# Optimization experiments

Hardware: AMD Instinct MI355X
Metric: run time of the kernel (lower is better)

## Reference

```python
import jax, jax.numpy as jnp
import numpy as np

N_NODES = 50000
N_EDGES = 800000
F_IN, F_HID, F_OUT = 128, 256, 128


def setup_inputs() -> dict:
    key = jax.random.key(0)
    ks = jax.random.split(key, 16)
    inp = {
        "x": jax.random.normal(ks[0], (N_NODES, F_IN), dtype=jnp.float32),
        "edge0": jax.random.randint(ks[1], (2, N_EDGES), 0, N_NODES, dtype=jnp.int64),
        "edge1": jax.random.randint(ks[2], (2, N_EDGES), 0, N_NODES, dtype=jnp.int64),
        "edge2": jax.random.randint(ks[3], (2, N_EDGES), 0, N_NODES, dtype=jnp.int64),
    }
    dims = [(F_IN, F_HID), (F_HID, F_HID), (F_HID, F_OUT)]
    for i, (di, do) in enumerate(dims):
        inp[f"Wl{i}"] = 0.02 * jax.random.normal(ks[4 + 3 * i], (di, do), dtype=jnp.float32)
        inp[f"bl{i}"] = jnp.zeros((do,), dtype=jnp.float32)
        inp[f"Wr{i}"] = 0.02 * jax.random.normal(ks[5 + 3 * i], (di, do), dtype=jnp.float32)
    return inp


def _sage_layer(x, src, dst, Wl, bl, Wr):
    # gather source features, mean-aggregate into destinations
    msg = x[src]                                            # [E, F]
    agg = jax.ops.segment_sum(msg, dst, num_segments=N_NODES)
    cnt = jax.ops.segment_sum(jnp.ones((src.shape[0], 1), x.dtype), dst,
                              num_segments=N_NODES)
    mean = agg / jnp.maximum(cnt, 1.0)
    # PyG SAGEConv: lin_l(aggr) + lin_r(x_self); lin_r has no bias
    return mean @ Wl + bl + x @ Wr


def reference(x, edge0, edge1, edge2, Wl0, bl0, Wr0, Wl1, bl1, Wr1, Wl2, bl2, Wr2):
    # vstack-swap + flow='target_to_source' == aggregate edge[0] -> edge[1]
    edges = [edge0, edge1, edge2]
    params = [(Wl0, bl0, Wr0), (Wl1, bl1, Wr1), (Wl2, bl2, Wr2)]
    h = x
    for e, (Wl, bl, Wr) in zip(edges, params):
        h = _sage_layer(h, e[0], e[1], Wl, bl, Wr)
        h = jax.nn.relu(h)
        # dropout skipped (eval mode)
    return h
```

## Files before the change

### kernel.cpp

```cpp
#include <hip/hip_runtime.h>
#include <hip/hip_bf16.h>
#include <stdint.h>

#define N_NODES 50000
#define N_EDGES 800000
#define NBG 196
#define MG 3125
#define MG64 782
#define EG 3125

typedef __attribute__((ext_vector_type(8))) short short8;
typedef __attribute__((ext_vector_type(4))) float floatx4;

__device__ __forceinline__ float bfbits2f(unsigned int u16) {
    union { unsigned int i; float f; } c; c.i = u16 << 16; return c.f;
}
__device__ __forceinline__ unsigned short f2bfbits(float f) {
    union { float f; unsigned int i; } c; c.f = f;
    unsigned int r = c.i + 0x7fffu + ((c.i >> 16) & 1u);
    return (unsigned short)(r >> 16);
}
__device__ __forceinline__ void acc8(float* a, uint4 v) {
    a[0] += bfbits2f(v.x & 0xffffu); a[1] += bfbits2f(v.x >> 16);
    a[2] += bfbits2f(v.y & 0xffffu); a[3] += bfbits2f(v.y >> 16);
    a[4] += bfbits2f(v.z & 0xffffu); a[5] += bfbits2f(v.z >> 16);
    a[6] += bfbits2f(v.w & 0xffffu); a[7] += bfbits2f(v.w >> 16);
}

__device__ __forceinline__ void count_body(
    int i, const int* __restrict__ e, int* __restrict__ rp, int f1)
{
    int dst = f1 ? e[2 * (N_EDGES + i)] : e[N_EDGES + i];
    atomicAdd(&rp[dst], 1);
}

__device__ __forceinline__ void fill_body(
    int i, const int* __restrict__ e, int* __restrict__ rp,
    const int* __restrict__ part, int* __restrict__ csr, int f1)
{
    int src = f1 ? e[2 * i] : e[i];
    int dst = f1 ? e[2 * (N_EDGES + i)] : e[N_EDGES + i];
    int pos = part[dst >> 8] + atomicAdd(&rp[dst], 1);
    csr[pos] = src;
}

__global__ __launch_bounds__(256) void mega1(
    const void* __restrict__ Wl0, const void* __restrict__ Wr0,
    const void* __restrict__ Wl1, const void* __restrict__ Wr1,
    const void* __restrict__ Wl2, const void* __restrict__ Wr2,
    const void* __restrict__ b0, const void* __restrict__ b1, const void* __restrict__ b2,
    unsigned short* __restrict__ wt,
    const void* __restrict__ x, unsigned short* __restrict__ xb,
    const int* __restrict__ e0,
    int* __restrict__ rp0, int* __restrict__ flagsOut)
{
    __shared__ int s_cnt[2];
    const int t = threadIdx.x;
    if (t < 2) s_cnt[t] = 0;
    __syncthreads();
    {
        unsigned short v = ((const unsigned short*)x)[2 * t];
        int ex = (v >> 7) & 0xff;
        unsigned long long m0 = __ballot(v == 0 || (ex >= 96 && ex <= 150));
        unsigned long long m1 = __ballot(e0[2 * t + 1] != 0);
        if ((t & 63) == 0) {
            atomicAdd(&s_cnt[0], (int)__popcll(m0));
            atomicAdd(&s_cnt[1], (int)__popcll(m1));
        }
    }
    __syncthreads();
    const int f0 = (s_cnt[0] < 200) ? 1 : 0;
    const int f1 = (s_cnt[1] < 128) ? 1 : 0;
    const int bid = blockIdx.x;

    if (bid == 10402) {
        if (t == 0) { flagsOut[0] = f0; flagsOut[1] = f1; }
        return;
    }
    if (bid >= 7277) {
        count_body((bid - 7277) * 256 + t, e0, rp0, f1);
        return;
    }
    if (bid >= 1027) {
        int i = (bid - 1027) * 256 + t;
        if (f0) {
            float4 v = ((const float4*)x)[i];
            uint2 o;
            o.x = (unsigned int)f2bfbits(v.x) | ((unsigned int)f2bfbits(v.y) << 16);
            o.y = (unsigned int)f2bfbits(v.z) | ((unsigned int)f2bfbits(v.w) << 16);
            ((uint2*)xb)[i] = o;
        } else {
            ((uint2*)xb)[i] = ((const uint2*)x)[i];
        }
        return;
    }
    if (bid >= 1024) {
        const void* bs = bid == 1024 ? b0 : (bid == 1025 ? b1 : b2);
        unsigned short* bd = wt + 262144 + (bid - 1024) * 256;
        int n = (bid == 1026) ? 128 : 256;
        if (t < n) bd[t] = f0 ? f2bfbits(((const float*)bs)[t]) : ((const unsigned short*)bs)[t];
        return;
    }
    const void* W; unsigned short* WT; int Nd, SK, KO, off;
    if (bid < 128)      { W = Wl0; WT = wt;          Nd = 256; off = bid;       SK = 256; KO = 0;   }
    else if (bid < 256) { W = Wr0; WT = wt;          Nd = 256; off = bid - 128; SK = 256; KO = 128; }
    else if (bid < 512) { W = Wl1; WT = wt + 65536;  Nd = 256; off = bid - 256; SK = 512; KO = 0;   }
    else if (bid < 768) { W = Wr1; WT = wt + 65536;  Nd = 256; off = bid - 512; SK = 512; KO = 256; }
    else if (bid < 896) { W = Wl2; WT = wt + 196608; Nd = 128; off = bid - 768; SK = 256; KO = 0;   }
    else                { W = Wr2; WT = wt + 229376; Nd = 128; off = bid - 896; SK = 256; KO = 0;   }
    int idx = off * 256 + t;
    int k = idx / Nd, n = idx - k * Nd;
    unsigned short v = f0 ? f2bfbits(((const float*)W)[idx]) : ((const unsigned short*)W)[idx];
    WT[n * SK + KO + k] = v;
}

__global__ __launch_bounds__(256) void scan_g(
    int* __restrict__ rp, int* __restrict__ part, int* __restrict__ ticket)
{
    __shared__ int sa[256], sb[256];
    __shared__ int lastBlk;
    const int b = blockIdx.x, t = threadIdx.x, idx = b * 256 + t;
    int v = (idx < N_NODES) ? rp[idx] : 0;
    sa[t] = v;
    __syncthreads();
    bool par = true;
#pragma unroll
    for (int off = 1; off < 256; off <<= 1) {
        if (par) { int x2 = sa[t] + (t >= off ? sa[t - off] : 0); sb[t] = x2; }
        else     { int x2 = sb[t] + (t >= off ? sb[t - off] : 0); sa[t] = x2; }
        par = !par;
        __syncthreads();
    }
    if (idx < N_NODES) rp[idx] = sa[t] - v;
    if (t == 255) part[b] = sa[255];
    __threadfence();
    if (t == 0) lastBlk = (atomicAdd(ticket, 1) == (int)gridDim.x - 1) ? 1 : 0;
    __syncthreads();
    if (!lastBlk) return;

    int pv = (t < NBG) ? atomicAdd(&part[t], 0) : 0;
    sa[t] = pv;
    __syncthreads();
    par = true;
#pragma unroll
    for (int off = 1; off < 256; off <<= 1) {
        if (par) { int x2 = sa[t] + (t >= off ? sa[t - off] : 0); sb[t] = x2; }
        else     { int x2 = sb[t] + (t >= off ? sb[t - off] : 0); sa[t] = x2; }
        par = !par;
        __syncthreads();
    }
    if (t < NBG) part[t] = sa[t] - pv;
}

__global__ __launch_bounds__(256) void fill_k(
    const int* __restrict__ e, int* __restrict__ rp, const int* __restrict__ part,
    int* __restrict__ csr, const int* __restrict__ flags)
{
    fill_body(blockIdx.x * 256 + threadIdx.x, e, rp, part, csr, flags[1]);
}

template<int K, int OSTR>
__global__ __launch_bounds__(256) void gath(
    const unsigned short* __restrict__ hin,
    const int* __restrict__ rp, const int* __restrict__ part,
    const int* __restrict__ csr_src,
    unsigned short* __restrict__ mout,
    const int* __restrict__ eN, int* __restrict__ rpN,
    const int* __restrict__ flags)
{
    constexpr int CH = K / 8;
    constexpr int CAP = 1024;
    __shared__ int sidx[CAP];
    __shared__ int srp[17];
    const int tid = threadIdx.x;
    if (blockIdx.x >= MG) {
        count_body((blockIdx.x - MG) * 256 + tid, eN, rpN, flags[1]);
        return;
    }
    const int m0 = blockIdx.x * 16;
    if (tid < 17) {
        int r0 = m0 + tid - 1;
        srp[tid] = (r0 < 0) ? 0 : rp[r0] + part[r0 >> 8];
    }
    __syncthreads();
    const int base = srp[0];
    const int total = srp[16] - base;
    const bool staged = total <= CAP;
    if (staged) {
        for (int i = tid; i < total; i += 256) sidx[i] = csr_src[base + i];
    }
    __syncthreads();

    for (int it = tid; it < 16 * CH; it += 256) {
        const int rr = it / CH;
        const int cc = it & (CH - 1);
        const int beg = srp[rr];
        const int deg = srp[rr + 1] - beg;
        const int begl = beg - base;
        float a[8], g[8];
#pragma unroll
        for (int v = 0; v < 8; ++v) { a[v] = 0.f; g[v] = 0.f; }
        const unsigned short* col = hin + cc * 8;
        auto run = [&](auto IDX) {
            int j = 0;
            for (; j + 7 < deg; j += 8) {
                int s0 = IDX(j),     s1 = IDX(j + 1), s2 = IDX(j + 2), s3 = IDX(j + 3);
                int s4 = IDX(j + 4), s5 = IDX(j + 5), s6 = IDX(j + 6), s7 = IDX(j + 7);
                uint4 v0 = *(const uint4*)(col + (size_t)s0 * K);
                uint4 v1 = *(const uint4*)(col + (size_t)s1 * K);
                uint4 v2 = *(const uint4*)(col + (size_t)s2 * K);
                uint4 v3 = *(const uint4*)(col + (size_t)s3 * K);
                uint4 v4 = *(const uint4*)(col + (size_t)s4 * K);
                uint4 v5 = *(const uint4*)(col + (size_t)s5 * K);
                uint4 v6 = *(const uint4*)(col + (size_t)s6 * K);
                uint4 v7 = *(const uint4*)(col + (size_t)s7 * K);
                acc8(a, v0); acc8(g, v1); acc8(a, v2); acc8(g, v3);
                acc8(a, v4); acc8(g, v5); acc8(a, v6); acc8(g, v7);
            }
            for (; j + 1 < deg; j += 2) {
                int s0 = IDX(j), s1 = IDX(j + 1);
                uint4 v0 = *(const uint4*)(col + (size_t)s0 * K);
                uint4 v1 = *(const uint4*)(col + (size_t)s1 * K);
                acc8(a, v0); acc8(g, v1);
            }
            if (j < deg) {
                uint4 v0 = *(const uint4*)(col + (size_t)IDX(j) * K);
                acc8(a, v0);
            }
        };
        if (staged) run([&](int j) { return sidx[begl + j]; });
        else        run([&](int j) { return csr_src[beg + j]; });
        const float inv = 1.0f / fmaxf((float)deg, 1.0f);
        short8 t8;
#pragma unroll
        for (int v = 0; v < 8; ++v) t8[v] = (short)f2bfbits((a[v] + g[v]) * inv);
        *(short8*)(mout + (size_t)(m0 + rr) * OSTR + cc * 8) = t8;
    }
}

template<int K>
__global__ __launch_bounds__(256) void gemmcat(
    const unsigned short* __restrict__ mean, int mstr,
    const unsigned short* __restrict__ self, int sstr,
    const unsigned short* __restrict__ WcatT,
    const unsigned short* __restrict__ bb,
    unsigned short* __restrict__ hout,
    const int* __restrict__ ef, int* __restrict__ rpf, const int* __restrict__ partf,
    int* __restrict__ csr, const int* __restrict__ flags)
{
    constexpr int KE = 2 * K;
    constexpr int KH = 256;
    constexpr int NKH = KE / KH;
    constexpr int LDA = KH + 8;
    __shared__ unsigned short A[64][LDA];
    const int tid = threadIdx.x;
    if (blockIdx.x >= MG64) {
        fill_body((blockIdx.x - MG64) * 256 + tid, ef, rpf, partf, csr, flags[1]);
        return;
    }
    const int m0 = blockIdx.x * 64;
    const int lane = tid & 63, wave = tid >> 6;
    const int r = lane & 15, quad = lane >> 4;

    floatx4 acc[4][4] = {};

#pragma unroll
    for (int kh = 0; kh < NKH; ++kh) {
        if (kh) __syncthreads();
        for (int i = tid; i < 64 * (KH / 8); i += 256) {
            const int row = i / (KH / 8);
            const int c8 = i - row * (KH / 8);
            int grow = m0 + row; if (grow >= N_NODES) grow = N_NODES - 1;
            const int gc = kh * KH + c8 * 8;
            const unsigned short* src = (gc < K)
                ? (mean + (size_t)grow * mstr + gc)
                : (self + (size_t)grow * sstr + (gc - K));
            *(uint4*)&A[row][c8 * 8] = *(const uint4*)src;
        }
        __syncthreads();
#pragma unroll
        for (int nti = 0; nti < 4; ++nti) {
            const int n0 = (wave + nti * 4) * 16;
            short8 bf[KH / 32];
            const unsigned short* bp = WcatT + (size_t)(n0 + r) * KE + kh * KH + quad * 8;
#pragma unroll
            for (int k0 = 0; k0 < KH / 32; ++k0) bf[k0] = *(const short8*)(bp + k0 * 32);
#pragma unroll
            for (int mt = 0; mt < 4; ++mt) {
#pragma unroll
                for (int k0 = 0; k0 < KH / 32; ++k0)
                    acc[nti][mt] = __builtin_amdgcn_mfma_f32_16x16x32_bf16(
                        *(const short8*)&A[mt * 16 + r][k0 * 32 + quad * 8],
                        bf[k0], acc[nti][mt], 0, 0, 0);
            }
        }
    }

#pragma unroll
    for (int nti = 0; nti < 4; ++nti) {
        const int ccol = (wave + nti * 4) * 16 + r;
        const float bv = bfbits2f(bb[ccol]);
#pragma unroll
        for (int mt = 0; mt < 4; ++mt) {
#pragma unroll
            for (int i = 0; i < 4; ++i) {
                const int row = m0 + mt * 16 + quad * 4 + i;
                float v = acc[nti][mt][i] + bv;
                v = v > 0.f ? v : 0.f;
                if (row < N_NODES) hout[(size_t)row * 256 + ccol] = f2bfbits(v);
            }
        }
    }
}

__global__ __launch_bounds__(256) void gemmL2(
    const unsigned short* __restrict__ A,
    const unsigned short* __restrict__ WT,
    unsigned short* __restrict__ out0,
    unsigned short* __restrict__ out1)
{
    __shared__ unsigned short As[64][264];
    const int tid = threadIdx.x;
    const int m0 = blockIdx.x * 64;
    for (int i = tid; i < 64 * 32; i += 256) {
        int rr = i >> 5, cc = i & 31;
        int row = m0 + rr; if (row >= N_NODES) row = N_NODES - 1;
        *(uint4*)&As[rr][cc * 8] = *(const uint4*)(A + (size_t)row * 256 + cc * 8);
    }
    __syncthreads();
    const int lane = tid & 63, wave = tid >> 6;
    const int r = lane & 15, quad = lane >> 4;

    for (int nt = wave; nt < 16; nt += 4) {
        const int n0 = nt * 16;
        short8 bf[8];
        const unsigned short* bp = WT + (size_t)(n0 + r) * 256 + quad * 8;
#pragma unroll
        for (int k0 = 0; k0 < 8; ++k0) bf[k0] = *(const short8*)(bp + k0 * 32);
        const int ccol = n0 + r;
#pragma unroll
        for (int mt = 0; mt < 4; ++mt) {
            floatx4 acc = {0.f, 0.f, 0.f, 0.f};
#pragma unroll
            for (int k0 = 0; k0 < 8; ++k0)
                acc = __builtin_amdgcn_mfma_f32_16x16x32_bf16(
                    *(const short8*)&As[mt * 16 + r][k0 * 32 + quad * 8], bf[k0], acc, 0, 0, 0);
#pragma unroll
            for (int i = 0; i < 4; ++i) {
                const int row = m0 + mt * 16 + quad * 4 + i;
                if (row < N_NODES) {
                    unsigned short v = f2bfbits(acc[i]);
                    if (ccol < 128) out0[(size_t)row * 128 + ccol] = v;
                    else            out1[(size_t)row * 128 + ccol - 128] = v;
                }
            }
        }
    }
}

__global__ __launch_bounds__(256) void agg2(
    const unsigned short* __restrict__ hl2,
    const unsigned short* __restrict__ hr2,
    const int* __restrict__ rp, const int* __restrict__ part,
    const int* __restrict__ csr_src,
    const unsigned short* __restrict__ bb,
    void* __restrict__ out,
    const int* __restrict__ flags)
{
    constexpr int K = 128, CAP = 3072;
    __shared__ int sidx[CAP];
    __shared__ int srp[17];
    const int tid = threadIdx.x;
    const int m0 = blockIdx.x * 16;
    if (tid < 17) {
        int r0 = m0 + tid - 1;
        srp[tid] = (r0 < 0) ? 0 : rp[r0] + part[r0 >> 8];
    }
    __syncthreads();
    const int base = srp[0];
    const int total = srp[16] - base;
    const bool staged = total <= CAP;
    if (staged) {
        for (int i = tid; i < total; i += 256) sidx[i] = csr_src[base + i];
    }
    __syncthreads();

    const int rr = tid >> 4;
    const int cc = tid & 15;
    const int beg = srp[rr];
    const int deg = srp[rr + 1] - beg;
    const int begl = beg - base;
    float a[8], g[8];
#pragma unroll
    for (int v = 0; v < 8; ++v) { a[v] = 0.f; g[v] = 0.f; }
    const unsigned short* col = hl2 + cc * 8;
    auto run = [&](auto IDX) {
        int j = 0;
        for (; j + 7 < deg; j += 8) {
            int s0 = IDX(j),     s1 = IDX(j + 1), s2 = IDX(j + 2), s3 = IDX(j + 3);
            int s4 = IDX(j + 4), s5 = IDX(j + 5), s6 = IDX(j + 6), s7 = IDX(j + 7);
            uint4 v0 = *(const uint4*)(col + (size_t)s0 * K);
            uint4 v1 = *(const uint4*)(col + (size_t)s1 * K);
            uint4 v2 = *(const uint4*)(col + (size_t)s2 * K);
            uint4 v3 = *(const uint4*)(col + (size_t)s3 * K);
            uint4 v4 = *(const uint4*)(col + (size_t)s4 * K);
            uint4 v5 = *(const uint4*)(col + (size_t)s5 * K);
            uint4 v6 = *(const uint4*)(col + (size_t)s6 * K);
            uint4 v7 = *(const uint4*)(col + (size_t)s7 * K);
            acc8(a, v0); acc8(g, v1); acc8(a, v2); acc8(g, v3);
            acc8(a, v4); acc8(g, v5); acc8(a, v6); acc8(g, v7);
        }
        for (; j + 1 < deg; j += 2) {
            int s0 = IDX(j), s1 = IDX(j + 1);
            uint4 v0 = *(const uint4*)(col + (size_t)s0 * K);
            uint4 v1 = *(const uint4*)(col + (size_t)s1 * K);
            acc8(a, v0); acc8(g, v1);
        }
        if (j < deg) {
            uint4 v0 = *(const uint4*)(col + (size_t)IDX(j) * K);
            acc8(a, v0);
        }
    };
    if (staged) run([&](int j) { return sidx[begl + j]; });
    else        run([&](int j) { return csr_src[beg + j]; });

    const float inv = 1.0f / fmaxf((float)deg, 1.0f);
    const size_t ro = (size_t)(m0 + rr) * K + cc * 8;
    uint4 hv = *(const uint4*)(hr2 + ro);
    uint4 bv = *(const uint4*)(bb + cc * 8);
    float h8[8], b8[8];
    h8[0] = bfbits2f(hv.x & 0xffffu); h8[1] = bfbits2f(hv.x >> 16);
    h8[2] = bfbits2f(hv.y & 0xffffu); h8[3] = bfbits2f(hv.y >> 16);
    h8[4] = bfbits2f(hv.z & 0xffffu); h8[5] = bfbits2f(hv.z >> 16);
    h8[6] = bfbits2f(hv.w & 0xffffu); h8[7] = bfbits2f(hv.w >> 16);
    b8[0] = bfbits2f(bv.x & 0xffffu); b8[1] = bfbits2f(bv.x >> 16);
    b8[2] = bfbits2f(bv.y & 0xffffu); b8[3] = bfbits2f(bv.y >> 16);
    b8[4] = bfbits2f(bv.z & 0xffffu); b8[5] = bfbits2f(bv.z >> 16);
    b8[6] = bfbits2f(bv.w & 0xffffu); b8[7] = bfbits2f(bv.w >> 16);
    float o8[8];
#pragma unroll
    for (int v = 0; v < 8; ++v) {
        float m = (a[v] + g[v]) * inv + b8[v] + h8[v];
        o8[v] = m > 0.f ? m : 0.f;
    }
    if (flags[0]) {
        float* op = (float*)out + ro;
        float4 o0 = { o8[0], o8[1], o8[2], o8[3] };
        float4 o1 = { o8[4], o8[5], o8[6], o8[7] };
        *(float4*)op = o0;
        *(float4*)(op + 4) = o1;
    } else {
        short8 t8;
#pragma unroll
        for (int v = 0; v < 8; ++v) t8[v] = (short)f2bfbits(o8[v]);
        *(short8*)((unsigned short*)out + ro) = t8;
    }
}

extern "C" void kernel_launch(void* const* d_in, const int* in_sizes, int n_in,
                              void* d_out, int out_size, void* d_ws, size_t ws_size,
                              hipStream_t stream) {
    const void* x  = d_in[0];
    const int* e[3] = { (const int*)d_in[1], (const int*)d_in[2], (const int*)d_in[3] };

    char* ws = (char*)d_ws;
    int* flags = (int*)ws;
    unsigned short* wt = (unsigned short*)(ws + 1024);
    unsigned short* bb0 = wt + 262144;
    unsigned short* bb1 = wt + 262400;
    unsigned short* bb2 = wt + 262656;
    int* rp3    = (int*)(ws + 526592);
    int* ticket = (int*)(ws + 1126592);
    int* part3  = (int*)(ws + 1126604);
    int* csr    = (int*)(ws + 1128960);
    unsigned short* hA = (unsigned short*)(ws + 4328960);
    unsigned short* hB = (unsigned short*)(ws + 29928960);
    unsigned short* xb  = hB;
    unsigned short* hl2 = hA;
    unsigned short* hr2 = hA + (size_t)N_NODES * 128;

    int* rp0 = rp3, * rp1 = rp3 + N_NODES, * rp2 = rp3 + 2 * N_NODES;
    int* pt0 = part3, * pt1 = part3 + NBG, * pt2 = part3 + 2 * NBG;

    hipMemsetAsync(rp3, 0, 600012, stream);
    mega1<<<10403, 256, 0, stream>>>(d_in[4], d_in[6], d_in[7], d_in[9],
                                     d_in[10], d_in[12], d_in[5], d_in[8], d_in[11],
                                     wt, x, xb, e[0], rp0, flags);
    scan_g<<<NBG, 256, 0, stream>>>(rp0, pt0, ticket + 0);
    fill_k<<<EG, 256, 0, stream>>>(e[0], rp0, pt0, csr, flags);
    gath<128, 256><<<MG + EG, 256, 0, stream>>>(xb, rp0, pt0, csr, hA,
                                                e[1], rp1, flags);
    scan_g<<<NBG, 256, 0, stream>>>(rp1, pt1, ticket + 1);
    gemmcat<128><<<MG64 + EG, 256, 0, stream>>>(hA, 256, xb, 128,
                                                wt, bb0, hA,
                                                e[1], rp1, pt1, csr, flags);
    gath<256, 256><<<MG + EG, 256, 0, stream>>>(hA, rp1, pt1, csr, hB,
                                                e[2], rp2, flags);
    scan_g<<<NBG, 256, 0, stream>>>(rp2, pt2, ticket + 2);
    gemmcat<256><<<MG64 + EG, 256, 0, stream>>>(hB, 256, hA, 256,
                                                wt + 65536, bb1, hB,
                                                e[2], rp2, pt2, csr, flags);
    gemmL2<<<MG64, 256, 0, stream>>>(hB, wt + 196608, hl2, hr2);
    agg2<<<MG, 256, 0, stream>>>(hl2, hr2, rp2, pt2, csr, bb2, d_out, flags);
}
```

Measured before the change: 593.0 us.

## Coarsen edge count/fill blocks to four edges per thread and front-load them

The side-work that builds the edge histogram and CSR now handles four edges per thread, which cuts those block counts from 3125 to 782. In the fused gather and GEMM kernels, these blocks are moved to the start of the grid so they are dispatched first and overlap with the main work. The GEMM A-tile K chunk is also halved from 256 to 128, which shrinks LDS use and may raise occupancy at the cost of more synchronisation steps. Fewer, heavier atomic-issuing blocks lower scheduling overhead but may reduce latency hiding.

```diff
diff --git a/kernel.cpp b/kernel.cpp
--- a/kernel.cpp
+++ b/kernel.cpp
@@ -7,7 +7,7 @@
 #define NBG 196
 #define MG 3125
 #define MG64 782
-#define EG 3125
+#define EG4 782
 
 typedef __attribute__((ext_vector_type(8))) short short8;
 typedef __attribute__((ext_vector_type(4))) float floatx4;
@@ -27,21 +27,33 @@
     a[6] += bfbits2f(v.w & 0xffffu); a[7] += bfbits2f(v.w >> 16);
 }
 
-__device__ __forceinline__ void count_body(
-    int i, const int* __restrict__ e, int* __restrict__ rp, int f1)
-{
-    int dst = f1 ? e[2 * (N_EDGES + i)] : e[N_EDGES + i];
-    atomicAdd(&rp[dst], 1);
-}
-
-__device__ __forceinline__ void fill_body(
-    int i, const int* __restrict__ e, int* __restrict__ rp,
+__device__ __forceinline__ void count4_body(
+    int blk, int tid, const int* __restrict__ e, int* __restrict__ rp, int f1)
+{
+#pragma unroll
+    for (int u = 0; u < 4; ++u) {
+        int i = blk * 1024 + u * 256 + tid;
+        if (i < N_EDGES) {
+            int dst = f1 ? e[2 * (N_EDGES + i)] : e[N_EDGES + i];
+            atomicAdd(&rp[dst], 1);
+        }
+    }
+}
+
+__device__ __forceinline__ void fill4_body(
+    int blk, int tid, const int* __restrict__ e, int* __restrict__ rp,
     const int* __restrict__ part, int* __restrict__ csr, int f1)
 {
-    int src = f1 ? e[2 * i] : e[i];
-    int dst = f1 ? e[2 * (N_EDGES + i)] : e[N_EDGES + i];
-    int pos = part[dst >> 8] + atomicAdd(&rp[dst], 1);
-    csr[pos] = src;
+#pragma unroll
+    for (int u = 0; u < 4; ++u) {
+        int i = blk * 1024 + u * 256 + tid;
+        if (i < N_EDGES) {
+            int src = f1 ? e[2 * i] : e[i];
+            int dst = f1 ? e[2 * (N_EDGES + i)] : e[N_EDGES + i];
+            int pos = part[dst >> 8] + atomicAdd(&rp[dst], 1);
+            csr[pos] = src;
+        }
+    }
 }
 
 __global__ __launch_bounds__(256) void mega1(
@@ -73,12 +85,12 @@
     const int f1 = (s_cnt[1] < 128) ? 1 : 0;
     const int bid = blockIdx.x;
 
-    if (bid == 10402) {
+    if (bid == 8059) {
         if (t == 0) { flagsOut[0] = f0; flagsOut[1] = f1; }
         return;
     }
     if (bid >= 7277) {
-        count_body((bid - 7277) * 256 + t, e0, rp0, f1);
+        count4_body(bid - 7277, t, e0, rp0, f1);
         return;
     }
     if (bid >= 1027) {
@@ -156,7 +168,7 @@
     const int* __restrict__ e, int* __restrict__ rp, const int* __restrict__ part,
     int* __restrict__ csr, const int* __restrict__ flags)
 {
-    fill_body(blockIdx.x * 256 + threadIdx.x, e, rp, part, csr, flags[1]);
+    fill4_body(blockIdx.x, threadIdx.x, e, rp, part, csr, flags[1]);
 }
 
 template<int K, int OSTR>
@@ -173,11 +185,11 @@
     __shared__ int sidx[CAP];
     __shared__ int srp[17];
     const int tid = threadIdx.x;
-    if (blockIdx.x >= MG) {
-        count_body((blockIdx.x - MG) * 256 + tid, eN, rpN, flags[1]);
+    if (blockIdx.x < EG4) {
+        count4_body(blockIdx.x, tid, eN, rpN, flags[1]);
         return;
     }
-    const int m0 = blockIdx.x * 16;
+    const int m0 = (blockIdx.x - EG4) * 16;
     if (tid < 17) {
         int r0 = m0 + tid - 1;
         srp[tid] = (r0 < 0) ? 0 : rp[r0] + part[r0 >> 8];
@@ -249,16 +261,16 @@
     int* __restrict__ csr, const int* __restrict__ flags)
 {
     constexpr int KE = 2 * K;
-    constexpr int KH = 256;
+    constexpr int KH = 128;
     constexpr int NKH = KE / KH;
     constexpr int LDA = KH + 8;
     __shared__ unsigned short A[64][LDA];
     const int tid = threadIdx.x;
-    if (blockIdx.x >= MG64) {
-        fill_body((blockIdx.x - MG64) * 256 + tid, ef, rpf, partf, csr, flags[1]);
+    if (blockIdx.x < EG4) {
+        fill4_body(blockIdx.x, tid, ef, rpf, partf, csr, flags[1]);
         return;
     }
-    const int m0 = blockIdx.x * 64;
+    const int m0 = (blockIdx.x - EG4) * 64;
     const int lane = tid & 63, wave = tid >> 6;
     const int r = lane & 15, quad = lane >> 4;
 
@@ -483,23 +495,23 @@
     int* pt0 = part3, * pt1 = part3 + NBG, * pt2 = part3 + 2 * NBG;
 
     hipMemsetAsync(rp3, 0, 600012, stream);
-    mega1<<<10403, 256, 0, stream>>>(d_in[4], d_in[6], d_in[7], d_in[9],
-                                     d_in[10], d_in[12], d_in[5], d_in[8], d_in[11],
-                                     wt, x, xb, e[0], rp0, flags);
+    mega1<<<8060, 256, 0, stream>>>(d_in[4], d_in[6], d_in[7], d_in[9],
+                                    d_in[10], d_in[12], d_in[5], d_in[8], d_in[11],
+                                    wt, x, xb, e[0], rp0, flags);
     scan_g<<<NBG, 256, 0, stream>>>(rp0, pt0, ticket + 0);
-    fill_k<<<EG, 256, 0, stream>>>(e[0], rp0, pt0, csr, flags);
-    gath<128, 256><<<MG + EG, 256, 0, stream>>>(xb, rp0, pt0, csr, hA,
-                                                e[1], rp1, flags);
+    fill_k<<<EG4, 256, 0, stream>>>(e[0], rp0, pt0, csr, flags);
+    gath<128, 256><<<EG4 + MG, 256, 0, stream>>>(xb, rp0, pt0, csr, hA,
+                                                 e[1], rp1, flags);
     scan_g<<<NBG, 256, 0, stream>>>(rp1, pt1, ticket + 1);
-    gemmcat<128><<<MG64 + EG, 256, 0, stream>>>(hA, 256, xb, 128,
-                                                wt, bb0, hA,
-                                                e[1], rp1, pt1, csr, flags);
-    gath<256, 256><<<MG + EG, 256, 0, stream>>>(hA, rp1, pt1, csr, hB,
-                                                e[2], rp2, flags);
+    gemmcat<128><<<EG4 + MG64, 256, 0, stream>>>(hA, 256, xb, 128,
+                                                 wt, bb0, hA,
+                                                 e[1], rp1, pt1, csr, flags);
+    gath<256, 256><<<EG4 + MG, 256, 0, stream>>>(hA, rp1, pt1, csr, hB,
+                                                 e[2], rp2, flags);
     scan_g<<<NBG, 256, 0, stream>>>(rp2, pt2, ticket + 2);
-    gemmcat<256><<<MG64 + EG, 256, 0, stream>>>(hB, 256, hA, 256,
-                                                wt + 65536, bb1, hB,
-                                                e[2], rp2, pt2, csr, flags);
+    gemmcat<256><<<EG4 + MG64, 256, 0, stream>>>(hB, 256, hA, 256,
+                                                 wt + 65536, bb1, hB,
+                                                 e[2], rp2, pt2, csr, flags);
     gemmL2<<<MG64, 256, 0, stream>>>(hB, wt + 196608, hl2, hr2);
     agg2<<<MG, 256, 0, stream>>>(hl2, hr2, rp2, pt2, csr, bb2, d_out, flags);
 }
```

After: 614.3 us. 3.6% more time.
